# Kernel optimization log

Hardware: AMD Instinct MI355X
Metric: run time of the kernel (lower is better)

Reference implementation:

```python
import jax, jax.numpy as jnp
import numpy as np

EPS = 1e-5

def _bn(x, s, b, m, v):
    # inference-mode BatchNorm2d over channel axis of NCHW
    return (x - m[None, :, None, None]) * jax.lax.rsqrt(v[None, :, None, None] + EPS) \
           * s[None, :, None, None] + b[None, :, None, None]

def _conv3(x, w):
    return jax.lax.conv_general_dilated(x, w, (1, 1), 'SAME',
                                        dimension_numbers=('NCHW', 'OIHW', 'NCHW'))

def _conv1(x, w, b):
    # 1x1 conv as einsum; w: [out_c, in_c]
    return jnp.einsum('oc,bchw->bohw', w, x) + b[None, :, None, None]

def _cca(f, qw, qb, kw, kb, vw, vb, gamma):
    # Criss-cross attention (faithful to source: no diagonal -inf masking, INF() unused there)
    B, C, H, W = f.shape
    q = _conv1(f, qw, qb)   # [B, C/8, H, W]
    k = _conv1(f, kw, kb)   # [B, C/8, H, W]
    v = _conv1(f, vw, vb)   # [B, C,   H, W]
    # energy along column (same w, all h') and row (same h, all w')
    eH = jnp.einsum('bchw,bciw->bhwi', q, k)            # [B,H,W,H]
    eW = jnp.einsum('bchw,bchj->bhwj', q, k)            # [B,H,W,W]
    att = jax.nn.softmax(jnp.concatenate([eH, eW], axis=3), axis=3)  # [B,H,W,H+W]
    aH, aW = att[..., :H], att[..., H:]
    oH = jnp.einsum('bhwi,bciw->bchw', aH, v)
    oW = jnp.einsum('bhwj,bchj->bchw', aW, v)
    return gamma * (oH + oW) + f


def setup_inputs() -> dict:
    key = jax.random.key(0)
    ks = iter(jax.random.split(key, 64))
    B, Cin, H, W = 8, 2048, 64, 64
    Ci, Cq, Co = 256, 32, 512
    rn = lambda s, sc=0.02: jax.random.normal(next(ks), s, jnp.float32) * sc
    ru = lambda s: jax.random.uniform(next(ks), s, jnp.float32)
    return {
        'x': jax.random.normal(next(ks), (B, Cin, H, W), jnp.float32),
        'recurrence': 2,
        'conva_w': rn((Ci, Cin, 3, 3)),
        'bn_a_s': ru((Ci,)), 'bn_a_b': rn((Ci,), 0.1), 'bn_a_m': rn((Ci,), 0.1), 'bn_a_v': ru((Ci,)),
        'q_w': rn((Cq, Ci)), 'q_b': rn((Cq,), 0.1),
        'k_w': rn((Cq, Ci)), 'k_b': rn((Cq,), 0.1),
        'v_w': rn((Ci, Ci)), 'v_b': rn((Ci,), 0.1),
        'cca_gamma': rn((1,), 1.0),
        'convb_w': rn((Ci, Ci, 3, 3)),
        'bn_b_s': ru((Ci,)), 'bn_b_b': rn((Ci,), 0.1), 'bn_b_m': rn((Ci,), 0.1), 'bn_b_v': ru((Ci,)),
        'sq_w': rn((Ci, Ci)), 'sq_b': rn((Ci,), 0.1),
        'bn_g_s': ru((Ci,)), 'bn_g_b': rn((Ci,), 0.1), 'bn_g_m': rn((Ci,), 0.1), 'bn_g_v': ru((Ci,)),
        'fc1_w': rn((Ci // 2, Ci)), 'fc1_b': rn((Ci // 2,), 0.1),
        'fc2_w': rn((Ci, Ci // 2)), 'fc2_b': rn((Ci,), 0.1),
        'bott_w': rn((Co, Cin + 2 * Ci, 3, 3)),
        'bn_t_s': ru((Co,)), 'bn_t_b': rn((Co,), 0.1), 'bn_t_m': rn((Co,), 0.1), 'bn_t_v': ru((Co,)),
    }


def reference(x, recurrence, conva_w, bn_a_s, bn_a_b, bn_a_m, bn_a_v,
              q_w, q_b, k_w, k_b, v_w, v_b, cca_gamma,
              convb_w, bn_b_s, bn_b_b, bn_b_m, bn_b_v,
              sq_w, sq_b, bn_g_s, bn_g_b, bn_g_m, bn_g_v,
              fc1_w, fc1_b, fc2_w, fc2_b,
              bott_w, bn_t_s, bn_t_b, bn_t_m, bn_t_v):
    out = _bn(_conv3(x, conva_w), bn_a_s, bn_a_b, bn_a_m, bn_a_v)
    # Global_Avg_Pooling (SE gating) on conva output
    fm = jax.nn.relu(_bn(_conv1(out, sq_w, sq_b), bn_g_s, bn_g_b, bn_g_m, bn_g_v))
    vec = fm.mean(axis=(-2, -1))                       # [B, Ci]
    h = jax.nn.relu(vec @ fc1_w.T + fc1_b)
    gate = jax.nn.sigmoid(h @ fc2_w.T + fc2_b)
    out_gap = out * gate[:, :, None, None]
    # recurrent criss-cross attention
    for _ in range(recurrence):
        out = _cca(out, q_w, q_b, k_w, k_b, v_w, v_b, cca_gamma)
    out = _bn(_conv3(out, convb_w), bn_b_s, bn_b_b, bn_b_m, bn_b_v)
    cat = jnp.concatenate([x, out, out_gap], axis=1)   # [B, Cin+2*Ci, H, W]
    return _bn(_conv3(cat, bott_w), bn_t_s, bn_t_b, bn_t_m, bn_t_v)
```

## Files before the change

### kernel.cpp

```cpp
#include <hip/hip_runtime.h>
#include <hip/hip_bf16.h>

typedef unsigned short u16;
typedef unsigned int u32;
typedef __attribute__((ext_vector_type(8))) short short8;
typedef __attribute__((ext_vector_type(8))) unsigned short u16x8;
typedef __attribute__((ext_vector_type(4))) unsigned short u16x4;
typedef __attribute__((ext_vector_type(4))) float f32x4;

#define BN_EPS 1e-5f
#define PADW 66
#define CATC 2560

__device__ __forceinline__ u16 f2b(float f) {
    __hip_bfloat16 h = __float2bfloat16(f);
    return *reinterpret_cast<u16*>(&h);
}
__device__ __forceinline__ float b2f(u16 u) {
    __hip_bfloat16 h;
    *reinterpret_cast<u16*>(&h) = u;
    return __bfloat162float(h);
}
__device__ __forceinline__ void async_copy16(void* lds, const void* g) {
    __builtin_amdgcn_global_load_lds((const __attribute__((address_space(1))) u32*)g,
                                     (__attribute__((address_space(3))) u32*)lds, 16, 0, 0);
}
__device__ __forceinline__ void fence_() { asm volatile("" ::: "memory"); }
__device__ __forceinline__ void barrier_() { fence_(); __builtin_amdgcn_s_barrier(); fence_(); }

template<int TAPS, int BN, int EPI, int CPT, int NTILES, int KSPLIT>
__global__ __launch_bounds__(512, 2)
void gemm8(const u16* __restrict__ Ag, int cstride,
           const u16* __restrict__ Bg, int ktot_full, int klen,
           const float* __restrict__ alpha, const float* __restrict__ beta,
           u16* __restrict__ outb, int ostride, int ochoff,
           float* __restrict__ outf, int nch)
{
    constexpr int WN   = BN / 4;
    constexpr int NSUB = WN / 16;
    constexpr int NQ   = NSUB / 2;
    constexpr int BLH  = BN / 128;
    constexpr int ASZ  = 256 * 128;
    constexpr int BSZ  = BN * 128;
    const int KT = klen / 64;

    extern __shared__ __align__(16) char smem[];
    char* smA = smem;
    char* smB = smem + 2 * ASZ;

    const int tid  = threadIdx.x;
    const int lane = tid & 63;
    const int wave = tid >> 6;
    const int wr = wave >> 2;
    const int wc = wave & 3;

    const int nwg = gridDim.x;
    const int wg  = blockIdx.x;
    const int swz = (wg & 7) * (nwg >> 3) + (wg >> 3);
    const int sel = swz % (NTILES * KSPLIT);
    const int m0  = (swz / (NTILES * KSPLIT)) * 256;
    const int n0  = (sel / KSPLIT) * BN;
    const int ks  = sel % KSPLIT;
    const int kstart = ks * klen;

    const int sr = tid >> 3;
    const int sc = tid & 7;
    const int scx8 = (sc ^ (sr & 7)) * 8;
    long baseAe[4];
#pragma unroll
    for (int j = 0; j < 4; ++j) {
        int p = m0 + j * 64 + sr;
        int b = p >> 12, h = (p >> 6) & 63, w = p & 63;
        long apix = (TAPS == 1) ? ((long)(b * PADW + h + 1) * PADW + (w + 1))
                                : ((long)(b * PADW + h) * PADW + w);
        baseAe[j] = apix * cstride + scx8;
    }
    long baseBe[2 * BLH];
#pragma unroll
    for (int h = 0; h < 2; ++h)
#pragma unroll
        for (int l = 0; l < BLH; ++l)
            baseBe[h * BLH + l] = (long)(n0 + h * (BN / 2) + l * 64 + sr) * ktot_full + scx8;

    auto stA = [&](int bsel, int h, long aoff) {
#pragma unroll
        for (int l = 0; l < 2; ++l) {
            const u16* g = Ag + baseAe[2 * h + l] + aoff;
            async_copy16(smA + bsel * ASZ + h * 16384 + l * 8192 + tid * 16, g);
        }
    };
    auto stB = [&](int bsel, int h, int k0) {
#pragma unroll
        for (int l = 0; l < BLH; ++l) {
            const u16* g = Bg + baseBe[h * BLH + l] + k0;
            async_copy16(smB + bsel * BSZ + h * (BSZ / 2) + l * 8192 + tid * 16, g);
        }
    };

    const int rsel  = lane & 15;
    const int cswz0 = (((lane >> 4)     ^ (lane & 7)) << 4);
    const int cswz1 = (((4 | (lane >> 4)) ^ (lane & 7)) << 4);

    f32x4 acc[8][NSUB] = {};
    short8 a[4][2], b0[NQ][2], b1[NQ][2];

    auto ldA = [&](int bsel, int mh) {
        const char* base = smA + bsel * ASZ + (wr * 128 + mh * 64 + rsel) * 128;
#pragma unroll
        for (int mi = 0; mi < 4; ++mi) {
            a[mi][0] = *(const short8*)(base + mi * 2048 + cswz0);
            a[mi][1] = *(const short8*)(base + mi * 2048 + cswz1);
        }
    };
    auto ldB = [&](int bsel, int nh, short8 (&bb)[NQ][2]) {
        const char* base = smB + bsel * BSZ + (wc * WN + nh * (WN / 2) + rsel) * 128;
#pragma unroll
        for (int nj = 0; nj < NQ; ++nj) {
            bb[nj][0] = *(const short8*)(base + nj * 2048 + cswz0);
            bb[nj][1] = *(const short8*)(base + nj * 2048 + cswz1);
        }
    };
    auto quad = [&](int MH, int NH, short8 (&bb)[NQ][2]) {
#pragma unroll
        for (int mi = 0; mi < 4; ++mi)
#pragma unroll
            for (int nj = 0; nj < NQ; ++nj)
#pragma unroll
                for (int kk = 0; kk < 2; ++kk)
                    acc[MH * 4 + mi][NH * NQ + nj] =
                        __builtin_amdgcn_mfma_f32_16x16x32_bf16(
                            a[mi][kk], bb[nj][kk], acc[MH * 4 + mi][NH * NQ + nj], 0, 0, 0);
    };

    const int tap0 = kstart / CPT;
    int c0_ = kstart - tap0 * CPT;
    int dx_ = tap0 % 3;
    long aoff_ = ((long)dx_ + (long)(tap0 / 3) * PADW) * cstride + c0_;
    auto adv = [&]() {
        c0_ += 64; aoff_ += 64;
        if (c0_ == CPT) {
            c0_ = 0; aoff_ += (long)cstride - CPT;
            if (++dx_ == 3) { dx_ = 0; aoff_ += (long)(PADW - 3) * cstride; }
        }
    };

    stA(0, 0, aoff_); stA(0, 1, aoff_); stB(0, 0, kstart); stB(0, 1, kstart);
    adv();
    stB(1, 0, kstart + 64); stB(1, 1, kstart + 64); stA(1, 0, aoff_); stA(1, 1, aoff_);
    long paoff = aoff_;
    adv();
    int skb = kstart + 128;

    if constexpr (BN == 256) asm volatile("s_waitcnt vmcnt(8)" ::: "memory");
    else                     asm volatile("s_waitcnt vmcnt(6)" ::: "memory");
    barrier_();

    for (int kt = 0; kt < KT; ++kt) {
        const int buf = kt & 1;
        ldA(buf, 0); ldB(buf, 0, b0);
        if (kt >= 1 && kt + 1 < KT) stA(buf ^ 1, 1, paoff);
        barrier_(); asm volatile("s_waitcnt lgkmcnt(0)" ::: "memory");
        __builtin_amdgcn_s_setprio(1); quad(0, 0, b0); __builtin_amdgcn_s_setprio(0);
        barrier_();
        ldB(buf, 1, b1);
        barrier_(); asm volatile("s_waitcnt lgkmcnt(0)" ::: "memory");
        __builtin_amdgcn_s_setprio(1); quad(0, 1, b1); __builtin_amdgcn_s_setprio(0);
        barrier_();
        ldA(buf, 1);
        if (kt + 2 < KT) stB(buf, 0, skb);
        barrier_(); asm volatile("s_waitcnt lgkmcnt(0)" ::: "memory");
        __builtin_amdgcn_s_setprio(1); quad(1, 0, b0); __builtin_amdgcn_s_setprio(0);
        barrier_();
        if (kt + 2 < KT) { stB(buf, 1, skb); stA(buf, 0, aoff_); }
        barrier_();
        __builtin_amdgcn_s_setprio(1); quad(1, 1, b1); __builtin_amdgcn_s_setprio(0);
        if (kt + 2 >= KT) {
            asm volatile("s_waitcnt vmcnt(0)" ::: "memory");
        } else if constexpr (BN == 256) {
            asm volatile("s_waitcnt vmcnt(6)" ::: "memory");
        } else {
            asm volatile("s_waitcnt vmcnt(4)" ::: "memory");
        }
        barrier_();
        paoff = aoff_;
        adv(); skb += 64;
    }

    const int nl = lane & 15, mq = lane >> 4;
#pragma unroll
    for (int s = 0; s < 8; ++s) {
#pragma unroll
        for (int nj = 0; nj < NSUB; ++nj) {
            int n = n0 + wc * WN + nj * 16 + nl;
            float al = (EPI == 4) ? 1.f : alpha[n];
            float be = (EPI == 4) ? 0.f : beta[n];
#pragma unroll
            for (int r = 0; r < 4; ++r) {
                int m = m0 + wr * 128 + s * 16 + mq * 4 + r;
                float v = acc[s][nj][r] * al + be;
                if (EPI == 0) {
                    int b = m >> 12, h = (m >> 6) & 63, w = m & 63;
                    long addr = ((long)(b * PADW + h + 1) * PADW + (w + 1)) * ostride + ochoff + n;
                    outb[addr] = f2b(v);
                } else if (EPI == 2) {
                    int b = m >> 12, h = (m >> 6) & 63, w = m & 63;
                    outf[((long)(b * nch + n) << 12) + (h * 64 + w)] = v;
                } else {
                    outf[(long)ks * ((long)32768 * nch) + (long)m * nch + n] = v;
                }
            }
        }
    }
}

__global__ void combine_k(const float* __restrict__ P,
                          const float* __restrict__ alpha, const float* __restrict__ beta,
                          u16* __restrict__ dst, int dstride, int choff)
{
    int t = threadIdx.x;
    int m = blockIdx.x * 4 + (t >> 6);
    int n = (t & 63) * 4;
    int b = m >> 12, h = (m >> 6) & 63, w = m & 63;
    f32x4 v0 = *(const f32x4*)&P[(long)m * 256 + n];
    f32x4 v1 = *(const f32x4*)&P[(long)32768 * 256 + (long)m * 256 + n];
    f32x4 al = *(const f32x4*)&alpha[n];
    f32x4 be = *(const f32x4*)&beta[n];
    u16x4 r;
#pragma unroll
    for (int i = 0; i < 4; ++i) r[i] = f2b((v0[i] + v1[i]) * al[i] + be[i]);
    *(u16x4*)&dst[((long)(b * PADW + h + 1) * PADW + (w + 1)) * dstride + choff + n] = r;
}

__global__ void border_k(u16* __restrict__ cat, u16* __restrict__ f0)
{
    int i = blockIdx.x;
    int b = i / 260, r = i - b * 260;
    int ph, pw;
    if (r < 66)       { ph = 0;        pw = r; }
    else if (r < 132) { ph = 65;       pw = r - 66; }
    else if (r < 196) { ph = r - 131;  pw = 0; }
    else              { ph = r - 195;  pw = 65; }
    long pix = (long)(b * PADW + ph) * PADW + pw;
    int t = threadIdx.x;
    u16x8 z = {};
    *(u16x8*)&cat[pix * CATC + t * 8] = z;
    if (t < 64) *(u16x8*)&cat[pix * CATC + 2048 + t * 8] = z;
    if (t < 32) *(u16x8*)&f0[pix * 256 + t * 8] = z;
}

template<int TAPS, int EPI>
__global__ __launch_bounds__(256, 2)
void gemm_conv(const u16* __restrict__ A, int cstride, int cpt,
               const u16* __restrict__ Bw, int ktot,
               const float* __restrict__ alpha, const float* __restrict__ beta,
               u16* __restrict__ outb, int ostride, int ochoff,
               float* __restrict__ outf, int n_total)
{
    __shared__ u16 As[128][32];
    __shared__ u16 Bs[128][32];
    __shared__ float red[128];

    const int tid  = threadIdx.x;
    const int lane = tid & 63;
    const int wave = tid >> 6;
    const int wr = wave >> 1, wc = wave & 1;
    const int m0 = blockIdx.y * 128;
    const int n0 = blockIdx.x * 128;

    long pixbase[2];
    long browk[2];
#pragma unroll
    for (int i = 0; i < 2; ++i) {
        int row = i * 64 + (tid >> 2);
        int p = m0 + row;
        int b = p >> 12, h = (p >> 6) & 63, w = p & 63;
        if (TAPS == 1) pixbase[i] = (long)(b * PADW + h + 1) * PADW + (w + 1);
        else           pixbase[i] = (long)(b * PADW + h) * PADW + w;
        browk[i] = (long)(n0 + row) * ktot;
    }
    const int chunk = (tid & 3) * 8;

    f32x4 acc[4][4] = {};

    const int steps = ktot / 32;
    int c0 = 0, dx = 0;
    long toff = 0;
    for (int s = 0; s < steps; ++s) {
        const int k0 = s * 32;
#pragma unroll
        for (int i = 0; i < 2; ++i) {
            const u16* ga = A + (pixbase[i] + ((TAPS == 1) ? 0 : toff)) * cstride + c0 + chunk;
            async_copy16((char*)(&As[0][0]) + i * 4096 + tid * 16, ga);
            const u16* gb = Bw + browk[i] + k0 + chunk;
            async_copy16((char*)(&Bs[0][0]) + i * 4096 + tid * 16, gb);
        }
        asm volatile("s_waitcnt vmcnt(0)" ::: "memory");
        __syncthreads();

        short8 af[4], bf[4];
#pragma unroll
        for (int x = 0; x < 4; ++x) {
            af[x] = *(const short8*)&As[wr * 64 + x * 16 + (lane & 15)][(lane >> 4) * 8];
            bf[x] = *(const short8*)&Bs[wc * 64 + x * 16 + (lane & 15)][(lane >> 4) * 8];
        }
#pragma unroll
        for (int mi = 0; mi < 4; ++mi)
#pragma unroll
            for (int ni = 0; ni < 4; ++ni)
                acc[mi][ni] = __builtin_amdgcn_mfma_f32_16x16x32_bf16(af[mi], bf[ni], acc[mi][ni], 0, 0, 0);
        __syncthreads();

        c0 += 32;
        if (TAPS > 1 && c0 == cpt) {
            c0 = 0; dx++; toff += 1;
            if (dx == 3) { dx = 0; toff += PADW - 3; }
        }
    }

    const int nl = lane & 15;
    const int mq = lane >> 4;

    if (EPI == 3) {
        if (tid < 128) red[tid] = 0.f;
        __syncthreads();
#pragma unroll
        for (int ni = 0; ni < 4; ++ni) {
            int ncol = wc * 64 + ni * 16 + nl;
            int n = n0 + ncol;
            float aa = alpha[n], bb = beta[n];
            float ssum = 0.f;
#pragma unroll
            for (int mi = 0; mi < 4; ++mi)
#pragma unroll
                for (int r = 0; r < 4; ++r)
                    ssum += fmaxf(acc[mi][ni][r] * aa + bb, 0.f);
            atomicAdd(&red[ncol], ssum);
        }
        __syncthreads();
        if (tid < 128) {
            int b = m0 >> 12;
            atomicAdd(&outf[b * 256 + n0 + tid], red[tid]);
        }
    } else {
#pragma unroll
        for (int mi = 0; mi < 4; ++mi) {
#pragma unroll
            for (int r = 0; r < 4; ++r) {
                int m = m0 + wr * 64 + mi * 16 + mq * 4 + r;
#pragma unroll
                for (int ni = 0; ni < 4; ++ni) {
                    int n = n0 + wc * 64 + ni * 16 + nl;
                    float v = acc[mi][ni][r] * alpha[n] + beta[n];
                    outb[(long)m * ostride + n] = f2b(v);
                }
            }
        }
    }
}

__global__ void xpad_k(const float* __restrict__ x, u16* __restrict__ cat)
{
    __shared__ float T[64][65];
    int bh = blockIdx.y;
    int b = bh >> 6, h = bh & 63;
    int c0 = blockIdx.x * 64;
    int t = threadIdx.x;
#pragma unroll
    for (int i = 0; i < 16; ++i) {
        int cl = i * 4 + (t >> 6);
        int w = t & 63;
        T[cl][w] = x[(((long)b * 2048 + c0 + cl) * 64 + h) * 64 + w];
    }
    __syncthreads();
#pragma unroll
    for (int i = 0; i < 16; ++i) {
        int wl = i * 4 + (t >> 6);
        int cl = t & 63;
        cat[((long)(b * PADW + h + 1) * PADW + (wl + 1)) * CATC + c0 + cl] = f2b(T[cl][wl]);
    }
}

__global__ void prep_w3(const float* __restrict__ w, u16* __restrict__ o, int O, int C)
{
    int idx = blockIdx.x * 256 + threadIdx.x;
    if (idx >= O * C) return;
    int oo = idx / C, c = idx - oo * C;
    const float* s = w + (long)idx * 9;
    long base = (long)oo * 9 * C + c;
#pragma unroll
    for (int t = 0; t < 9; ++t) o[base + (long)t * C] = f2b(s[t]);
}

__global__ void prep_qkv(const float* __restrict__ qw, const float* __restrict__ kw,
                         const float* __restrict__ vw, u16* __restrict__ o)
{
    int idx = blockIdx.x * 256 + threadIdx.x;
    int n = idx >> 8, c = idx & 255;
    float v;
    if (n < 32) v = qw[n * 256 + c];
    else if (n < 64) v = kw[(n - 32) * 256 + c];
    else if (n < 320) v = vw[(n - 64) * 256 + c];
    else v = 0.f;
    o[idx] = f2b(v);
}

__global__ void prep_cast(const float* __restrict__ w, u16* __restrict__ o, int n)
{
    int i = blockIdx.x * 256 + threadIdx.x;
    if (i < n) o[i] = f2b(w[i]);
}

__global__ void prep_ab(const float* as, const float* ab, const float* am, const float* av,
                        const float* gs, const float* gb, const float* gm, const float* gv, const float* sqb,
                        const float* bs, const float* bb, const float* bm, const float* bv,
                        const float* ts, const float* tb, const float* tm, const float* tv,
                        const float* qb, const float* kb, const float* vb,
                        float* Aa, float* Ba_, float* Ag, float* Bg, float* Ab2, float* Bb2,
                        float* At, float* Bt, float* Aq, float* Bq)
{
    int i = blockIdx.x * 256 + threadIdx.x;
    if (i < 256) { float al = as[i] * rsqrtf(av[i] + BN_EPS); Aa[i] = al; Ba_[i] = ab[i] - am[i] * al; }
    else if (i < 512) { int n = i - 256; float al = gs[n] * rsqrtf(gv[n] + BN_EPS); Ag[n] = al; Bg[n] = gb[n] - gm[n] * al + sqb[n] * al; }
    else if (i < 768) { int n = i - 512; float al = bs[n] * rsqrtf(bv[n] + BN_EPS); Ab2[n] = al; Bb2[n] = bb[n] - bm[n] * al; }
    else if (i < 1280) { int n = i - 768; float al = ts[n] * rsqrtf(tv[n] + BN_EPS); At[n] = al; Bt[n] = tb[n] - tm[n] * al; }
    else if (i < 1664) { int n = i - 1280; Aq[n] = 1.f; Bq[n] = (n < 32) ? qb[n] : (n < 64) ? kb[n - 32] : (n < 320) ? vb[n - 64] : 0.f; }
}

__global__ void gate_k(const float* __restrict__ vacc, const float* __restrict__ fc1w,
                       const float* __restrict__ fc1b, const float* __restrict__ fc2w,
                       const float* __restrict__ fc2b, float* __restrict__ gate)
{
    __shared__ float v[256], hbuf[128];
    int b = blockIdx.x, t = threadIdx.x;
    v[t] = vacc[b * 256 + t] * (1.f / 4096.f);
    __syncthreads();
    if (t < 128) {
        float s = fc1b[t];
        for (int c = 0; c < 256; ++c) s += v[c] * fc1w[t * 256 + c];
        hbuf[t] = fmaxf(s, 0.f);
    }
    __syncthreads();
    float s = fc2b[t];
    for (int j = 0; j < 128; ++j) s += hbuf[j] * fc2w[t * 128 + j];
    gate[b * 256 + t] = 1.f / (1.f + __expf(-s));
}

__global__ void gap_k(const u16* __restrict__ f0, const float* __restrict__ gate, u16* __restrict__ cat)
{
    int p = blockIdx.x, t = threadIdx.x;
    int b = p >> 12, h = (p >> 6) & 63, w = p & 63;
    long ppad = (long)(b * PADW + h + 1) * PADW + (w + 1);
    float f = b2f(f0[ppad * 256 + t]);
    cat[ppad * CATC + 2304 + t] = f2b(f * gate[b * 256 + t]);
}

__global__ void gram_k(const u16* __restrict__ qkv, float* eH, float* eW)
{
    __shared__ u16 Qs[64][32];
    __shared__ u16 Ks[64][32];
    int g = blockIdx.x;
    int mode = g >> 9;
    int bx = g & 511;
    int b = bx >> 6, s = bx & 63;
    float* e = mode ? eW : eH;
    int tid = threadIdx.x, lane = tid & 63, wave = tid >> 6;
    {
        int r = tid >> 2, ch = (tid & 3) * 8;
        long pix = (mode == 0) ? ((long)(b * 64 + r) * 64 + s) : ((long)(b * 64 + s) * 64 + r);
        const u16* gp = qkv + pix * 384;
        *(u16x8*)&Qs[r][ch] = *(const u16x8*)(gp + ch);
        *(u16x8*)&Ks[r][ch] = *(const u16x8*)(gp + 32 + ch);
    }
    __syncthreads();
    f32x4 acc[4] = {};
    short8 a = *(const short8*)&Qs[wave * 16 + (lane & 15)][(lane >> 4) * 8];
#pragma unroll
    for (int ni = 0; ni < 4; ++ni) {
        short8 bb = *(const short8*)&Ks[ni * 16 + (lane & 15)][(lane >> 4) * 8];
        acc[ni] = __builtin_amdgcn_mfma_f32_16x16x32_bf16(a, bb, acc[ni], 0, 0, 0);
    }
#pragma unroll
    for (int ni = 0; ni < 4; ++ni)
#pragma unroll
        for (int r = 0; r < 4; ++r) {
            int row = wave * 16 + (lane >> 4) * 4 + r;
            int col = ni * 16 + (lane & 15);
            long pix = (mode == 0) ? ((long)(b * 64 + row) * 64 + s) : ((long)(b * 64 + s) * 64 + row);
            e[pix * 64 + col] = acc[ni][r];
        }
}

__global__ void softmax_k(const float* __restrict__ eH, const float* __restrict__ eW,
                          u16* __restrict__ aH, u16* __restrict__ aW)
{
    long row = blockIdx.x * 4 + (threadIdx.x >> 6);
    int lane = threadIdx.x & 63;
    float v0 = eH[row * 64 + lane];
    float v1 = eW[row * 64 + lane];
    float m = fmaxf(v0, v1);
#pragma unroll
    for (int off = 32; off; off >>= 1) m = fmaxf(m, __shfl_xor(m, off));
    float e0 = __expf(v0 - m), e1 = __expf(v1 - m);
    float s = e0 + e1;
#pragma unroll
    for (int off = 32; off; off >>= 1) s += __shfl_xor(s, off);
    float inv = 1.f / s;
    aH[row * 64 + lane] = f2b(e0 * inv);
    aW[row * 64 + lane] = f2b(e1 * inv);
}

__global__ __launch_bounds__(256, 2)
void oh_k(const u16* __restrict__ aH, const u16* __restrict__ qkv, float* __restrict__ oHb)
{
    __shared__ float Al[64][68];
    __shared__ u16 Vl[64][264];
    int bx = blockIdx.x;
    int b = bx >> 6, w = bx & 63;
    int t = threadIdx.x;
#pragma unroll
    for (int pass = 0; pass < 2; ++pass) {
        int r = pass * 32 + (t >> 3);
        int ch = (t & 7) * 8;
        u16x8 v = *(const u16x8*)(aH + ((long)(b * 64 + r) * 64 + w) * 64 + ch);
        f32x4 s0, s1;
#pragma unroll
        for (int u = 0; u < 4; ++u) { s0[u] = b2f(v[u]); s1[u] = b2f(v[4 + u]); }
        *(f32x4*)&Al[r][ch] = s0;
        *(f32x4*)&Al[r][ch + 4] = s1;
    }
#pragma unroll
    for (int pass = 0; pass < 8; ++pass) {
        int i = pass * 8 + (t >> 5);
        int ch = (t & 31) * 8;
        *(u16x8*)&Vl[i][ch] = *(const u16x8*)(qkv + ((long)(b * 64 + i) * 64 + w) * 384 + 64 + ch);
    }
    __syncthreads();
    int hb = (t >> 5) * 8, cb = (t & 31) * 8;
    float acc[8][8] = {};
    for (int i = 0; i < 64; ++i) {
        float av[8], vv[8];
        u16x8 v8 = *(const u16x8*)&Vl[i][cb];
#pragma unroll
        for (int u = 0; u < 8; ++u) av[u] = Al[hb + u][i];
#pragma unroll
        for (int u = 0; u < 8; ++u) vv[u] = b2f(v8[u]);
#pragma unroll
        for (int u = 0; u < 8; ++u)
#pragma unroll
            for (int x = 0; x < 8; ++x)
                acc[u][x] += av[u] * vv[x];
    }
#pragma unroll
    for (int u = 0; u < 8; ++u) {
        long base = ((long)(b * 64 + hb + u) * 64 + w) * 256 + cb;
        f32x4 s0, s1;
#pragma unroll
        for (int x = 0; x < 4; ++x) { s0[x] = acc[u][x]; s1[x] = acc[u][4 + x]; }
        *(f32x4*)&oHb[base] = s0;
        *(f32x4*)&oHb[base + 4] = s1;
    }
}

__global__ __launch_bounds__(256, 2)
void ow_k(const u16* __restrict__ aW, const u16* __restrict__ qkv, const float* __restrict__ oHb,
          const u16* __restrict__ fin, u16* __restrict__ fout, const float* __restrict__ gamma_p)
{
    __shared__ float Al[64][68];
    __shared__ u16 Vl[64][264];
    int bx = blockIdx.x;
    int b = bx >> 6, h = bx & 63;
    int t = threadIdx.x;
    float gamma = gamma_p[0];
#pragma unroll
    for (int pass = 0; pass < 2; ++pass) {
        int r = pass * 32 + (t >> 3);
        int ch = (t & 7) * 8;
        u16x8 v = *(const u16x8*)(aW + ((long)(b * 64 + h) * 64 + r) * 64 + ch);
        f32x4 s0, s1;
#pragma unroll
        for (int u = 0; u < 4; ++u) { s0[u] = b2f(v[u]); s1[u] = b2f(v[4 + u]); }
        *(f32x4*)&Al[r][ch] = s0;
        *(f32x4*)&Al[r][ch + 4] = s1;
    }
#pragma unroll
    for (int pass = 0; pass < 8; ++pass) {
        int j = pass * 8 + (t >> 5);
        int ch = (t & 31) * 8;
        *(u16x8*)&Vl[j][ch] = *(const u16x8*)(qkv + ((long)(b * 64 + h) * 64 + j) * 384 + 64 + ch);
    }
    __syncthreads();
    int wb = (t >> 5) * 8, cb = (t & 31) * 8;
    float acc[8][8] = {};
    for (int j = 0; j < 64; ++j) {
        float av[8], vv[8];
        u16x8 v8 = *(const u16x8*)&Vl[j][cb];
#pragma unroll
        for (int u = 0; u < 8; ++u) av[u] = Al[wb + u][j];
#pragma unroll
        for (int u = 0; u < 8; ++u) vv[u] = b2f(v8[u]);
#pragma unroll
        for (int u = 0; u < 8; ++u)
#pragma unroll
            for (int x = 0; x < 8; ++x)
                acc[u][x] += av[u] * vv[x];
    }
#pragma unroll
    for (int u = 0; u < 8; ++u) {
        int w = wb + u;
        long pix = ((long)(b * 64 + h) * 64 + w) * 256 + cb;
        long pp = ((long)(b * PADW + h + 1) * PADW + (w + 1)) * 256 + cb;
        u16x8 f8 = *(const u16x8*)&fin[pp];
        f32x4 o0 = *(const f32x4*)&oHb[pix];
        f32x4 o1 = *(const f32x4*)&oHb[pix + 4];
        u16x8 r8;
#pragma unroll
        for (int x = 0; x < 8; ++x) {
            float o = acc[u][x] + ((x < 4) ? o0[x] : o1[x - 4]);
            r8[x] = f2b(gamma * o + b2f(f8[x]));
        }
        *(u16x8*)&fout[pp] = r8;
    }
}

extern "C" void kernel_launch(void* const* d_in, const int* in_sizes, int n_in,
                              void* d_out, int out_size, void* d_ws, size_t ws_size,
                              hipStream_t stream)
{
    const float* x       = (const float*)d_in[0];
    const float* conva_w = (const float*)d_in[2];
    const float* bn_a_s  = (const float*)d_in[3];
    const float* bn_a_b  = (const float*)d_in[4];
    const float* bn_a_m  = (const float*)d_in[5];
    const float* bn_a_v  = (const float*)d_in[6];
    const float* q_w     = (const float*)d_in[7];
    const float* q_b     = (const float*)d_in[8];
    const float* k_w     = (const float*)d_in[9];
    const float* k_b     = (const float*)d_in[10];
    const float* v_w     = (const float*)d_in[11];
    const float* v_b     = (const float*)d_in[12];
    const float* gamma   = (const float*)d_in[13];
    const float* convb_w = (const float*)d_in[14];
    const float* bn_b_s  = (const float*)d_in[15];
    const float* bn_b_b  = (const float*)d_in[16];
    const float* bn_b_m  = (const float*)d_in[17];
    const float* bn_b_v  = (const float*)d_in[18];
    const float* sq_w    = (const float*)d_in[19];
    const float* sq_b    = (const float*)d_in[20];
    const float* bn_g_s  = (const float*)d_in[21];
    const float* bn_g_b  = (const float*)d_in[22];
    const float* bn_g_m  = (const float*)d_in[23];
    const float* bn_g_v  = (const float*)d_in[24];
    const float* fc1_w   = (const float*)d_in[25];
    const float* fc1_b   = (const float*)d_in[26];
    const float* fc2_w   = (const float*)d_in[27];
    const float* fc2_b   = (const float*)d_in[28];
    const float* bott_w  = (const float*)d_in[29];
    const float* bn_t_s  = (const float*)d_in[30];
    const float* bn_t_b  = (const float*)d_in[31];
    const float* bn_t_m  = (const float*)d_in[32];
    const float* bn_t_v  = (const float*)d_in[33];

    char* ws = (char*)d_ws;
    size_t off = 0;
    auto alloc = [&](size_t bytes) { char* p = ws + off; off += (bytes + 255) & ~(size_t)255; return p; };

    u16*   CAT  = (u16*)  alloc((size_t)8 * PADW * PADW * CATC * 2);
    u16*   F0   = (u16*)  alloc((size_t)8 * PADW * PADW * 256 * 2);
    u16*   F1   = (u16*)  alloc((size_t)8 * PADW * PADW * 256 * 2);
    size_t cca_off = off;
    u16*   QKV  = (u16*)  alloc((size_t)32768 * 384 * 2);
    float* EH   = (float*)alloc((size_t)32768 * 64 * 4);
    float* EWb  = (float*)alloc((size_t)32768 * 64 * 4);
    u16*   AH   = (u16*)  alloc((size_t)32768 * 64 * 2);
    u16*   AW   = (u16*)  alloc((size_t)32768 * 64 * 2);
    float* OHB  = (float*)alloc((size_t)32768 * 256 * 4);
    float* P    = (float*)(ws + cca_off);
    u16*   WA   = (u16*)  alloc((size_t)256 * 18432 * 2);
    u16*   WB   = (u16*)  alloc((size_t)256 * 2304 * 2);
    u16*   WT   = (u16*)  alloc((size_t)512 * 23040 * 2);
    u16*   WQKV = (u16*)  alloc((size_t)384 * 256 * 2);
    u16*   WSQ  = (u16*)  alloc((size_t)256 * 256 * 2);
    float* Aa   = (float*)alloc(256 * 4);
    float* Ba_  = (float*)alloc(256 * 4);
    float* Ag   = (float*)alloc(256 * 4);
    float* Bg   = (float*)alloc(256 * 4);
    float* Ab2  = (float*)alloc(256 * 4);
    float* Bb2  = (float*)alloc(256 * 4);
    float* At   = (float*)alloc(512 * 4);
    float* Bt   = (float*)alloc(512 * 4);
    float* Aq   = (float*)alloc(384 * 4);
    float* Bq   = (float*)alloc(384 * 4);
    float* VACC = (float*)alloc(8 * 256 * 4);
    float* GATE = (float*)alloc(8 * 256 * 4);

    hipFuncSetAttribute((const void*)gemm8<9, 256, 4, 2048, 1, 2>,
                        hipFuncAttributeMaxDynamicSharedMemorySize, 131072);
    hipFuncSetAttribute((const void*)gemm8<9, 256, 4, 256, 1, 2>,
                        hipFuncAttributeMaxDynamicSharedMemorySize, 131072);
    hipFuncSetAttribute((const void*)gemm8<9, 256, 2, 2560, 2, 1>,
                        hipFuncAttributeMaxDynamicSharedMemorySize, 131072);

    hipMemsetAsync(VACC, 0, 8 * 256 * 4, stream);

    border_k<<<8 * 260, 256, 0, stream>>>(CAT, F0);
    prep_w3<<<(256 * 2048 + 255) / 256, 256, 0, stream>>>(conva_w, WA, 256, 2048);
    prep_w3<<<(256 * 256 + 255) / 256, 256, 0, stream>>>(convb_w, WB, 256, 256);
    prep_w3<<<(512 * 2560 + 255) / 256, 256, 0, stream>>>(bott_w, WT, 512, 2560);
    prep_qkv<<<384, 256, 0, stream>>>(q_w, k_w, v_w, WQKV);
    prep_cast<<<256, 256, 0, stream>>>(sq_w, WSQ, 65536);
    prep_ab<<<7, 256, 0, stream>>>(bn_a_s, bn_a_b, bn_a_m, bn_a_v,
                                   bn_g_s, bn_g_b, bn_g_m, bn_g_v, sq_b,
                                   bn_b_s, bn_b_b, bn_b_m, bn_b_v,
                                   bn_t_s, bn_t_b, bn_t_m, bn_t_v,
                                   q_b, k_b, v_b,
                                   Aa, Ba_, Ag, Bg, Ab2, Bb2, At, Bt, Aq, Bq);
    xpad_k<<<dim3(32, 512), 256, 0, stream>>>(x, CAT);

    gemm8<9, 256, 4, 2048, 1, 2><<<256, 512, 131072, stream>>>(
        CAT, CATC, WA, 18432, 9216, Aa, Ba_, nullptr, 0, 0, P, 256);
    combine_k<<<8192, 256, 0, stream>>>(P, Aa, Ba_, F0, 256, 0);

    gemm_conv<1, 3><<<dim3(2, 256), 256, 0, stream>>>(F0, 256, 256, WSQ, 256, Ag, Bg, nullptr, 0, 0, VACC, 0);
    gate_k<<<8, 256, 0, stream>>>(VACC, fc1_w, fc1_b, fc2_w, fc2_b, GATE);
    gap_k<<<32768, 256, 0, stream>>>(F0, GATE, CAT);

    for (int rec = 0; rec < 2; ++rec) {
        u16* fin = rec ? F1 : F0;
        u16* fout = rec ? F0 : F1;
        gemm_conv<1, 1><<<dim3(3, 256), 256, 0, stream>>>(fin, 256, 256, WQKV, 256, Aq, Bq, QKV, 384, 0, nullptr, 0);
        gram_k<<<1024, 256, 0, stream>>>(QKV, EH, EWb);
        softmax_k<<<8192, 256, 0, stream>>>(EH, EWb, AH, AW);
        oh_k<<<512, 256, 0, stream>>>(AH, QKV, OHB);
        ow_k<<<512, 256, 0, stream>>>(AW, QKV, OHB, fin, fout, gamma);
    }

    gemm8<9, 256, 4, 256, 1, 2><<<256, 512, 131072, stream>>>(
        F0, 256, WB, 2304, 1152, Ab2, Bb2, nullptr, 0, 0, P, 256);
    combine_k<<<8192, 256, 0, stream>>>(P, Ab2, Bb2, CAT, CATC, 2048);

    gemm8<9, 256, 2, 2560, 2, 1><<<256, 512, 131072, stream>>>(
        CAT, CATC, WT, 23040, 23040, At, Bt, nullptr, 0, 0, (float*)d_out, 512);
}
```

Measured before the change: 1.232 ms.

## Merge GEMM sub-phases to cut barriers and vectorize x padding transpose

The conv GEMM main loop now loads both B fragments at once and runs two quads per phase. This halves the number of barrier and lgkmcnt waits per k-tile, and the next tile's LDS stores are issued together. The xpad transpose kernel now does 16-byte float4 global reads and 8-wide bf16 packed writes through a 68-padded LDS tile. The fused phases raise register pressure because both B fragments are live at once. The removed explicit lgkmcnt waits may also leave LDS reads unsynchronized unless the compiler inserts them.

```diff
diff --git a/kernel.cpp b/kernel.cpp
--- a/kernel.cpp
+++ b/kernel.cpp
@@ -157,23 +157,19 @@
 
     for (int kt = 0; kt < KT; ++kt) {
         const int buf = kt & 1;
-        ldA(buf, 0); ldB(buf, 0, b0);
+        ldA(buf, 0); ldB(buf, 0, b0); ldB(buf, 1, b1);
         if (kt >= 1 && kt + 1 < KT) stA(buf ^ 1, 1, paoff);
-        barrier_(); asm volatile("s_waitcnt lgkmcnt(0)" ::: "memory");
-        __builtin_amdgcn_s_setprio(1); quad(0, 0, b0); __builtin_amdgcn_s_setprio(0);
         barrier_();
-        ldB(buf, 1, b1);
-        barrier_(); asm volatile("s_waitcnt lgkmcnt(0)" ::: "memory");
-        __builtin_amdgcn_s_setprio(1); quad(0, 1, b1); __builtin_amdgcn_s_setprio(0);
+        __builtin_amdgcn_s_setprio(1);
+        quad(0, 0, b0); quad(0, 1, b1);
+        __builtin_amdgcn_s_setprio(0);
         barrier_();
         ldA(buf, 1);
-        if (kt + 2 < KT) stB(buf, 0, skb);
-        barrier_(); asm volatile("s_waitcnt lgkmcnt(0)" ::: "memory");
-        __builtin_amdgcn_s_setprio(1); quad(1, 0, b0); __builtin_amdgcn_s_setprio(0);
+        if (kt + 2 < KT) { stB(buf, 0, skb); stB(buf, 1, skb); stA(buf, 0, aoff_); }
         barrier_();
-        if (kt + 2 < KT) { stB(buf, 1, skb); stA(buf, 0, aoff_); }
-        barrier_();
-        __builtin_amdgcn_s_setprio(1); quad(1, 1, b1); __builtin_amdgcn_s_setprio(0);
+        __builtin_amdgcn_s_setprio(1);
+        quad(1, 0, b0); quad(1, 1, b1);
+        __builtin_amdgcn_s_setprio(0);
         if (kt + 2 >= KT) {
             asm volatile("s_waitcnt vmcnt(0)" ::: "memory");
         } else if constexpr (BN == 256) {
@@ -360,23 +356,28 @@
 
 __global__ void xpad_k(const float* __restrict__ x, u16* __restrict__ cat)
 {
-    __shared__ float T[64][65];
+    __shared__ float T[64][68];
     int bh = blockIdx.y;
     int b = bh >> 6, h = bh & 63;
     int c0 = blockIdx.x * 64;
     int t = threadIdx.x;
-#pragma unroll
-    for (int i = 0; i < 16; ++i) {
-        int cl = i * 4 + (t >> 6);
-        int w = t & 63;
-        T[cl][w] = x[(((long)b * 2048 + c0 + cl) * 64 + h) * 64 + w];
+    const float* xb = x + (((long)b * 2048 + c0) * 64 + h) * 64;
+#pragma unroll
+    for (int i = 0; i < 4; ++i) {
+        int idx = i * 256 + t;
+        int c = idx >> 4, wq = (idx & 15) * 4;
+        *(f32x4*)&T[c][wq] = *(const f32x4*)&xb[(long)c * 4096 + wq];
     }
     __syncthreads();
-#pragma unroll
-    for (int i = 0; i < 16; ++i) {
-        int wl = i * 4 + (t >> 6);
-        int cl = t & 63;
-        cat[((long)(b * PADW + h + 1) * PADW + (wl + 1)) * CATC + c0 + cl] = f2b(T[cl][wl]);
+    long pbase = ((long)(b * PADW + h + 1) * PADW + 1) * CATC + c0;
+#pragma unroll
+    for (int j = 0; j < 2; ++j) {
+        int idx = j * 256 + t;
+        int w = idx >> 3, cg = (idx & 7) * 8;
+        u16x8 r;
+#pragma unroll
+        for (int u = 0; u < 8; ++u) r[u] = f2b(T[cg + u][w]);
+        *(u16x8*)&cat[pbase + (long)w * CATC + cg] = r;
     }
 }
 
```

Measured after the change: 1.253 ms. Within noise of the previous version (+1.7%).
